# Kernel tuning notes

Hardware: AMD Instinct MI355X
Metric: run time of the kernel (lower is better)

## Reference

```python
import jax, jax.numpy as jnp
import numpy as np

MAX_DISTANCE = 10
N_OUT = 8


def setup_inputs() -> dict:
    key = jax.random.key(0)
    k1, k2 = jax.random.split(key)
    B, N = 32, 512
    adjacency = jax.random.uniform(k1, (B, N, N), dtype=jnp.float32)
    node_mask = jnp.ones((B, N), dtype=bool)
    emb = jax.random.normal(k2, (MAX_DISTANCE + 2, N_OUT), dtype=jnp.float32)
    return {"adjacency": adjacency, "node_mask": node_mask, "emb": emb}


def _shortest_path_indices(adjacency, node_mask):
    """All-pairs BFS distances up to MAX_DISTANCE via frontier matmuls.

    Returns int32 (B, N, N): d in [0, MAX_DISTANCE] if reachable within
    MAX_DISTANCE hops, else MAX_DISTANCE + 1 (also for invalid node pairs).
    """
    B, N, _ = adjacency.shape
    adj = adjacency > 0.5
    adj = adj | jnp.swapaxes(adj, -1, -2)  # symmetrize
    valid_pair = node_mask[:, :, None] & node_mask[:, None, :]
    adj = (adj & valid_pair).astype(jnp.float32)  # (B, N, N)

    eye = jnp.eye(N, dtype=bool)[None]
    reach0 = eye & valid_pair  # dist 0 only on valid diagonal
    dist0 = jnp.where(reach0, 0, MAX_DISTANCE + 1).astype(jnp.int32)

    def step(carry, t):
        reach, dist = carry
        expanded = jnp.matmul(reach.astype(jnp.float32), adj) > 0  # one BFS hop
        newly = expanded & ~reach
        dist = jnp.where(newly, t.astype(jnp.int32), dist)
        return (reach | newly, dist), None

    (_, dist), _ = jax.lax.scan(step, (reach0, dist0), jnp.arange(1, MAX_DISTANCE + 1))
    return dist


def reference(adjacency, node_mask, emb):
    dist = _shortest_path_indices(adjacency, node_mask)  # (B, N, N)
    return emb[dist]  # (B, N, N, n_out)
```

## Files before the change

kernel.cpp:

```cpp
#include <hip/hip_runtime.h>

#define NODES 512
#define WORDS 16
#define NBATCH 32
#define SENTINEL 11
#define NEMB 12
#define NOUT 8
#define G 2

__global__ void __launch_bounds__(256)
pack_bits(const float* __restrict__ A, const int* __restrict__ mask,
          unsigned int* __restrict__ bitA) {
    const int tid = blockIdx.x * 256 + threadIdx.x;
    const int t = threadIdx.x;
    const int w = tid & 15;
    const int i = (tid >> 4) & 511;
    const int b = tid >> 13;

    __shared__ unsigned int s_mw[WORDS];
    {
        bool m0 = mask[b * NODES + t] != 0;
        bool m1 = mask[b * NODES + 256 + t] != 0;
        unsigned long long b0 = __ballot(m0);
        unsigned long long b1 = __ballot(m1);
        if ((t & 63) == 0) {
            int wv = t >> 6;
            s_mw[2 * wv]         = (unsigned int)b0;
            s_mw[2 * wv + 1]     = (unsigned int)(b0 >> 32);
            s_mw[8 + 2 * wv]     = (unsigned int)b1;
            s_mw[8 + 2 * wv + 1] = (unsigned int)(b1 >> 32);
        }
    }

    const float4* p = (const float4*)(A + (size_t)tid * 32);
    unsigned int bits = 0;
#pragma unroll
    for (int q = 0; q < 8; ++q) {
        float4 v = p[q];
        bits |= (v.x > 0.5f ? 1u : 0u) << (4 * q);
        bits |= (v.y > 0.5f ? 1u : 0u) << (4 * q + 1);
        bits |= (v.z > 0.5f ? 1u : 0u) << (4 * q + 2);
        bits |= (v.w > 0.5f ? 1u : 0u) << (4 * q + 3);
    }
    __syncthreads();
    bool rv = (s_mw[i >> 5] >> (i & 31)) & 1u;
    bitA[tid] = rv ? (bits & s_mw[w]) : 0u;
}

__global__ void __launch_bounds__(256)
symmetrize(const unsigned int* __restrict__ bitA, unsigned int* __restrict__ adjb) {
    int tid = blockIdx.x * 256 + threadIdx.x;
    int w = tid & 15;
    int i = (tid >> 4) & 511;
    int b = tid >> 13;
    const unsigned int* base = bitA + (size_t)b * NODES * WORDS;
    unsigned int word = base[i * WORDS + w];
    unsigned int t = 0;
    int iw = i >> 5, ib = i & 31;
#pragma unroll
    for (int k = 0; k < 32; ++k) {
        t |= ((base[(32 * w + k) * WORDS + iw] >> ib) & 1u) << k;
    }
    adjb[tid] = word | t;
}

__global__ void __launch_bounds__(512, 8)
bfs_store(const unsigned int* __restrict__ adjb, const int* __restrict__ mask,
          const float* __restrict__ emb, float4* __restrict__ out4) {
    const int i0 = blockIdx.x * G;
    const int b = blockIdx.y;
    const int j = threadIdx.x;

    __shared__ unsigned int s_f[2][G][WORDS];
    __shared__ unsigned int s_state[2][8];
    __shared__ unsigned int s_dist[NODES];
    __shared__ __align__(16) float s_emb[NEMB * NOUT];

    if (j < NEMB * NOUT) s_emb[j] = emb[j];

    const uint4* rowp = (const uint4*)(adjb + ((size_t)b * NODES + j) * WORDS);
    uint4 ar0 = rowp[0], ar1 = rowp[1], ar2 = rowp[2], ar3 = rowp[3];

    const bool valid_j = (mask[b * NODES + j] != 0);

    if (j < G * WORDS) {
        int s = j >> 4, w = j & 15;
        int i = i0 + s;
        bool v = (mask[b * NODES + i] != 0);
        s_f[0][s][w] = (v && (i >> 5) == w) ? (1u << (i & 31)) : 0u;
    }

    unsigned int dists = 0x0B0Bu;
    unsigned int reachm = 0;
#pragma unroll
    for (int s = 0; s < G; ++s) {
        if ((j == i0 + s) && valid_j) {
            dists &= ~(0xffu << (8 * s));
            reachm |= 1u << s;
        }
    }
    __syncthreads();

    int p = 0;
    for (int t = 1; t <= 10; ++t) {
        unsigned int newm = 0;
#pragma unroll
        for (int s = 0; s < G; ++s) {
            const uint4* f4 = (const uint4*)s_f[p][s];
            uint4 f0 = f4[0], f1 = f4[1], f2 = f4[2], f3 = f4[3];
            unsigned int hit =
                (ar0.x & f0.x) | (ar0.y & f0.y) | (ar0.z & f0.z) | (ar0.w & f0.w) |
                (ar1.x & f1.x) | (ar1.y & f1.y) | (ar1.z & f1.z) | (ar1.w & f1.w) |
                (ar2.x & f2.x) | (ar2.y & f2.y) | (ar2.z & f2.z) | (ar2.w & f2.w) |
                (ar3.x & f3.x) | (ar3.y & f3.y) | (ar3.z & f3.z) | (ar3.w & f3.w);
            if (hit && !((reachm >> s) & 1u)) newm |= 1u << s;
        }
        unsigned long long bal0 = __ballot(newm & 1u);
        unsigned long long bal1 = __ballot((newm >> 1) & 1u);
        bool alldone = (((reachm | newm) == 3u) || !valid_j);
        unsigned long long balD = __ballot(alldone);
        if ((j & 63) == 0) {
            int wv = j >> 6;
            s_f[p ^ 1][0][2 * wv]     = (unsigned int)bal0;
            s_f[p ^ 1][0][2 * wv + 1] = (unsigned int)(bal0 >> 32);
            s_f[p ^ 1][1][2 * wv]     = (unsigned int)bal1;
            s_f[p ^ 1][1][2 * wv + 1] = (unsigned int)(bal1 >> 32);
            s_state[p ^ 1][wv] = (((bal0 | bal1) != 0ull) ? 1u : 0u) |
                                 ((balD == ~0ull) ? 2u : 0u);
        }
#pragma unroll
        for (int s = 0; s < G; ++s) {
            if ((newm >> s) & 1u)
                dists = (dists & ~(0xffu << (8 * s))) | ((unsigned int)t << (8 * s));
        }
        reachm |= newm;
        __syncthreads();
        p ^= 1;
        unsigned int anyw = 0, donew = 2;
#pragma unroll
        for (int wv = 0; wv < 8; ++wv) {
            unsigned int st = s_state[p][wv];
            anyw |= st;
            donew &= st;
        }
        if (!(anyw & 1u) || (donew & 2u)) break;
    }

    s_dist[j] = dists;
    __syncthreads();

    const float4* e4 = (const float4*)s_emb;
    unsigned int dw0 = s_dist[j >> 1];
    unsigned int dw1 = s_dist[256 + (j >> 1)];
    const int half = j & 1;
    size_t base0 = ((size_t)b * NODES + i0) * (NODES * NOUT / 4);
#pragma unroll
    for (int s = 0; s < G; ++s) {
        int d0 = (dw0 >> (8 * s)) & 0xff;
        int d1 = (dw1 >> (8 * s)) & 0xff;
        out4[base0 + (size_t)s * 1024 + j]       = e4[2 * d0 + half];
        out4[base0 + (size_t)s * 1024 + 512 + j] = e4[2 * d1 + half];
    }
}

extern "C" void kernel_launch(void* const* d_in, const int* in_sizes, int n_in,
                              void* d_out, int out_size, void* d_ws, size_t ws_size,
                              hipStream_t stream) {
    const float* adjacency = (const float*)d_in[0];
    const int* node_mask = (const int*)d_in[1];
    const float* emb = (const float*)d_in[2];
    float4* out4 = (float4*)d_out;

    unsigned int* bitA = (unsigned int*)d_ws;
    unsigned int* adjb = bitA + (size_t)NBATCH * NODES * WORDS;

    pack_bits<<<1024, 256, 0, stream>>>(adjacency, node_mask, bitA);
    symmetrize<<<1024, 256, 0, stream>>>(bitA, adjb);
    bfs_store<<<dim3(NODES / G, NBATCH), 512, 0, stream>>>(adjb, node_mask, emb, out4);
}
```

Measured before the change: 79.14 us.

## Compute BFS hops one and two directly from source row, one source per block

After: 80.42 us. Within noise of the previous version (+1.6%).

```diff
diff --git a/kernel.cpp b/kernel.cpp
--- a/kernel.cpp
+++ b/kernel.cpp
@@ -6,7 +6,6 @@
 #define SENTINEL 11
 #define NEMB 12
 #define NOUT 8
-#define G 2
 
 __global__ void __launch_bounds__(256)
 pack_bits(const float* __restrict__ A, const int* __restrict__ mask,
@@ -64,102 +63,137 @@
     adjb[tid] = word | t;
 }
 
-__global__ void __launch_bounds__(512, 8)
+__global__ void __launch_bounds__(256, 8)
 bfs_store(const unsigned int* __restrict__ adjb, const int* __restrict__ mask,
           const float* __restrict__ emb, float4* __restrict__ out4) {
-    const int i0 = blockIdx.x * G;
+    const int i = blockIdx.x;
     const int b = blockIdx.y;
-    const int j = threadIdx.x;
-
-    __shared__ unsigned int s_f[2][G][WORDS];
-    __shared__ unsigned int s_state[2][8];
-    __shared__ unsigned int s_dist[NODES];
+    const int t = threadIdx.x;
+    const int cA = t, cB = t + 256;
+
+    __shared__ unsigned int s_rowi[WORDS];
+    __shared__ unsigned int s_f[2][WORDS];
+    __shared__ unsigned int s_state[2][4];
+    __shared__ unsigned char s_d8[NODES];
     __shared__ __align__(16) float s_emb[NEMB * NOUT];
 
-    if (j < NEMB * NOUT) s_emb[j] = emb[j];
-
-    const uint4* rowp = (const uint4*)(adjb + ((size_t)b * NODES + j) * WORDS);
-    uint4 ar0 = rowp[0], ar1 = rowp[1], ar2 = rowp[2], ar3 = rowp[3];
-
-    const bool valid_j = (mask[b * NODES + j] != 0);
-
-    if (j < G * WORDS) {
-        int s = j >> 4, w = j & 15;
-        int i = i0 + s;
-        bool v = (mask[b * NODES + i] != 0);
-        s_f[0][s][w] = (v && (i >> 5) == w) ? (1u << (i & 31)) : 0u;
-    }
-
-    unsigned int dists = 0x0B0Bu;
-    unsigned int reachm = 0;
-#pragma unroll
-    for (int s = 0; s < G; ++s) {
-        if ((j == i0 + s) && valid_j) {
-            dists &= ~(0xffu << (8 * s));
-            reachm |= 1u << s;
+    if (t < NEMB * NOUT) s_emb[t] = emb[t];
+
+    const unsigned int* Ab = adjb + (size_t)b * NODES * WORDS;
+    if (t < 4) ((uint4*)s_rowi)[t] = ((const uint4*)(Ab + (size_t)i * WORDS))[t];
+
+    const bool valid_i = (mask[b * NODES + i] != 0);
+    const bool validA  = (mask[b * NODES + cA] != 0);
+    const bool validB  = (mask[b * NODES + cB] != 0);
+
+    const uint4* rA = (const uint4*)(Ab + (size_t)cA * WORDS);
+    const uint4* rB = (const uint4*)(Ab + (size_t)cB * WORDS);
+
+    __syncthreads();
+
+    uint4 i0 = ((const uint4*)s_rowi)[0], i1 = ((const uint4*)s_rowi)[1],
+          i2 = ((const uint4*)s_rowi)[2], i3 = ((const uint4*)s_rowi)[3];
+
+    uint4 a0 = rA[0], a1 = rA[1], a2 = rA[2], a3 = rA[3];
+    unsigned int hA =
+        (a0.x & i0.x) | (a0.y & i0.y) | (a0.z & i0.z) | (a0.w & i0.w) |
+        (a1.x & i1.x) | (a1.y & i1.y) | (a1.z & i1.z) | (a1.w & i1.w) |
+        (a2.x & i2.x) | (a2.y & i2.y) | (a2.z & i2.z) | (a2.w & i2.w) |
+        (a3.x & i3.x) | (a3.y & i3.y) | (a3.z & i3.z) | (a3.w & i3.w);
+    uint4 b0 = rB[0], b1 = rB[1], b2 = rB[2], b3 = rB[3];
+    unsigned int hB =
+        (b0.x & i0.x) | (b0.y & i0.y) | (b0.z & i0.z) | (b0.w & i0.w) |
+        (b1.x & i1.x) | (b1.y & i1.y) | (b1.z & i1.z) | (b1.w & i1.w) |
+        (b2.x & i2.x) | (b2.y & i2.y) | (b2.z & i2.z) | (b2.w & i2.w) |
+        (b3.x & i3.x) | (b3.y & i3.y) | (b3.z & i3.z) | (b3.w & i3.w);
+
+    unsigned int bit1A = (s_rowi[cA >> 5] >> (cA & 31)) & 1u;
+    unsigned int bit1B = (s_rowi[cB >> 5] >> (cB & 31)) & 1u;
+
+    int dA = (cA == i && valid_i) ? 0 : (bit1A ? 1 : (hA ? 2 : SENTINEL));
+    int dB = (cB == i && valid_i) ? 0 : (bit1B ? 1 : (hB ? 2 : SENTINEL));
+
+    {
+        unsigned long long fA = __ballot(dA == 2);
+        unsigned long long fB = __ballot(dB == 2);
+        bool doneP = ((dA <= 2) || !validA) && ((dB <= 2) || !validB);
+        unsigned long long balD = __ballot(doneP);
+        int w = t >> 6;
+        if ((t & 63) == 0) {
+            s_f[0][2 * w]         = (unsigned int)fA;
+            s_f[0][2 * w + 1]     = (unsigned int)(fA >> 32);
+            s_f[0][8 + 2 * w]     = (unsigned int)fB;
+            s_f[0][8 + 2 * w + 1] = (unsigned int)(fB >> 32);
+            s_state[0][w] = (((fA | fB) != 0ull) ? 1u : 0u) |
+                            ((balD == ~0ull) ? 2u : 0u);
         }
     }
     __syncthreads();
-
-    int p = 0;
-    for (int t = 1; t <= 10; ++t) {
-        unsigned int newm = 0;
-#pragma unroll
-        for (int s = 0; s < G; ++s) {
-            const uint4* f4 = (const uint4*)s_f[p][s];
-            uint4 f0 = f4[0], f1 = f4[1], f2 = f4[2], f3 = f4[3];
-            unsigned int hit =
-                (ar0.x & f0.x) | (ar0.y & f0.y) | (ar0.z & f0.z) | (ar0.w & f0.w) |
-                (ar1.x & f1.x) | (ar1.y & f1.y) | (ar1.z & f1.z) | (ar1.w & f1.w) |
-                (ar2.x & f2.x) | (ar2.y & f2.y) | (ar2.z & f2.z) | (ar2.w & f2.w) |
-                (ar3.x & f3.x) | (ar3.y & f3.y) | (ar3.z & f3.z) | (ar3.w & f3.w);
-            if (hit && !((reachm >> s) & 1u)) newm |= 1u << s;
+    unsigned int anyw = 0, donew = 2;
+#pragma unroll
+    for (int wv = 0; wv < 4; ++wv) {
+        unsigned int st = s_state[0][wv];
+        anyw |= st; donew &= st;
+    }
+
+    if ((anyw & 1u) && !(donew & 2u)) {
+        bool reachA = (dA != SENTINEL), reachB = (dB != SENTINEL);
+        int p = 0;
+        const int w = t >> 6;
+        for (int tt = 3; tt <= 10; ++tt) {
+            uint4 f0 = ((const uint4*)s_f[p])[0], f1 = ((const uint4*)s_f[p])[1],
+                  f2 = ((const uint4*)s_f[p])[2], f3 = ((const uint4*)s_f[p])[3];
+            uint4 x0 = rA[0], x1 = rA[1], x2 = rA[2], x3 = rA[3];
+            unsigned int hitA =
+                (x0.x & f0.x) | (x0.y & f0.y) | (x0.z & f0.z) | (x0.w & f0.w) |
+                (x1.x & f1.x) | (x1.y & f1.y) | (x1.z & f1.z) | (x1.w & f1.w) |
+                (x2.x & f2.x) | (x2.y & f2.y) | (x2.z & f2.z) | (x2.w & f2.w) |
+                (x3.x & f3.x) | (x3.y & f3.y) | (x3.z & f3.z) | (x3.w & f3.w);
+            uint4 y0 = rB[0], y1 = rB[1], y2 = rB[2], y3 = rB[3];
+            unsigned int hitB =
+                (y0.x & f0.x) | (y0.y & f0.y) | (y0.z & f0.z) | (y0.w & f0.w) |
+                (y1.x & f1.x) | (y1.y & f1.y) | (y1.z & f1.z) | (y1.w & f1.w) |
+                (y2.x & f2.x) | (y2.y & f2.y) | (y2.z & f2.z) | (y2.w & f2.w) |
+                (y3.x & f3.x) | (y3.y & f3.y) | (y3.z & f3.z) | (y3.w & f3.w);
+            bool newA = hitA && !reachA;
+            bool newB = hitB && !reachB;
+            unsigned long long nA = __ballot(newA);
+            unsigned long long nB = __ballot(newB);
+            bool dn = (reachA || newA || !validA) && (reachB || newB || !validB);
+            unsigned long long bD = __ballot(dn);
+            if ((t & 63) == 0) {
+                s_f[p ^ 1][2 * w]         = (unsigned int)nA;
+                s_f[p ^ 1][2 * w + 1]     = (unsigned int)(nA >> 32);
+                s_f[p ^ 1][8 + 2 * w]     = (unsigned int)nB;
+                s_f[p ^ 1][8 + 2 * w + 1] = (unsigned int)(nB >> 32);
+                s_state[p ^ 1][w] = (((nA | nB) != 0ull) ? 1u : 0u) |
+                                    ((bD == ~0ull) ? 2u : 0u);
+            }
+            if (newA) { reachA = true; dA = tt; }
+            if (newB) { reachB = true; dB = tt; }
+            __syncthreads();
+            p ^= 1;
+            unsigned int aw = 0, dw = 2;
+#pragma unroll
+            for (int wv = 0; wv < 4; ++wv) {
+                unsigned int st = s_state[p][wv];
+                aw |= st; dw &= st;
+            }
+            if (!(aw & 1u) || (dw & 2u)) break;
         }
-        unsigned long long bal0 = __ballot(newm & 1u);
-        unsigned long long bal1 = __ballot((newm >> 1) & 1u);
-        bool alldone = (((reachm | newm) == 3u) || !valid_j);
-        unsigned long long balD = __ballot(alldone);
-        if ((j & 63) == 0) {
-            int wv = j >> 6;
-            s_f[p ^ 1][0][2 * wv]     = (unsigned int)bal0;
-            s_f[p ^ 1][0][2 * wv + 1] = (unsigned int)(bal0 >> 32);
-            s_f[p ^ 1][1][2 * wv]     = (unsigned int)bal1;
-            s_f[p ^ 1][1][2 * wv + 1] = (unsigned int)(bal1 >> 32);
-            s_state[p ^ 1][wv] = (((bal0 | bal1) != 0ull) ? 1u : 0u) |
-                                 ((balD == ~0ull) ? 2u : 0u);
-        }
-#pragma unroll
-        for (int s = 0; s < G; ++s) {
-            if ((newm >> s) & 1u)
-                dists = (dists & ~(0xffu << (8 * s))) | ((unsigned int)t << (8 * s));
-        }
-        reachm |= newm;
-        __syncthreads();
-        p ^= 1;
-        unsigned int anyw = 0, donew = 2;
-#pragma unroll
-        for (int wv = 0; wv < 8; ++wv) {
-            unsigned int st = s_state[p][wv];
-            anyw |= st;
-            donew &= st;
-        }
-        if (!(anyw & 1u) || (donew & 2u)) break;
-    }
-
-    s_dist[j] = dists;
+    }
+
+    s_d8[cA] = (unsigned char)dA;
+    s_d8[cB] = (unsigned char)dB;
     __syncthreads();
 
     const float4* e4 = (const float4*)s_emb;
-    unsigned int dw0 = s_dist[j >> 1];
-    unsigned int dw1 = s_dist[256 + (j >> 1)];
-    const int half = j & 1;
-    size_t base0 = ((size_t)b * NODES + i0) * (NODES * NOUT / 4);
-#pragma unroll
-    for (int s = 0; s < G; ++s) {
-        int d0 = (dw0 >> (8 * s)) & 0xff;
-        int d1 = (dw1 >> (8 * s)) & 0xff;
-        out4[base0 + (size_t)s * 1024 + j]       = e4[2 * d0 + half];
-        out4[base0 + (size_t)s * 1024 + 512 + j] = e4[2 * d1 + half];
+    size_t base = ((size_t)b * NODES + i) * (NODES * NOUT / 4);
+#pragma unroll
+    for (int q = 0; q < 4; ++q) {
+        int k = t + 256 * q;
+        int d = s_d8[k >> 1];
+        out4[base + k] = e4[2 * d + (k & 1)];
     }
 }
 
@@ -176,5 +210,5 @@
 
     pack_bits<<<1024, 256, 0, stream>>>(adjacency, node_mask, bitA);
     symmetrize<<<1024, 256, 0, stream>>>(bitA, adjb);
-    bfs_store<<<dim3(NODES / G, NBATCH), 512, 0, stream>>>(adjb, node_mask, emb, out4);
-}
+    bfs_store<<<dim3(NODES, NBATCH), 256, 0, stream>>>(adjb, node_mask, emb, out4);
+}
```
